# Kernel optimization log

Hardware: AMD Instinct MI355X
Metric: run time of the kernel (lower is better)

Reference implementation:

```python
import math
import jax, jax.numpy as jnp
import numpy as np

GROUPS = 8

def setup_inputs() -> dict:
    key = jax.random.key(0)
    ks = jax.random.split(key, 6)
    N, H, W, C = 8, 128, 128, 512
    s = 1.0 / math.sqrt(C)
    return {
        "x": jax.random.normal(ks[0], (N, H, W, C), dtype=jnp.float32),
        "Wq": jax.random.normal(ks[1], (C, C), dtype=jnp.float32) * s,
        "Wk": jax.random.normal(ks[2], (C, C), dtype=jnp.float32) * s,
        "Wv": jax.random.normal(ks[3], (C, C), dtype=jnp.float32) * s,
        "Wo": jax.random.normal(ks[4], (C, C), dtype=jnp.float32) * s,
        "bo": jnp.zeros((C,), dtype=jnp.float32),
    }

def reference(x, Wq, Wk, Wv, Wo, bo):
    # width=False: attend along H axis -> permute to [N, W, H, C]
    x = jnp.transpose(x, (0, 2, 1, 3))
    N, W, H, C = x.shape
    g = GROUPS
    gp = C // g  # group_planes (head dim)
    xr = x.reshape(N * W, H, C)
    # torch nn.Linear: y = x @ W^T
    q = (xr @ Wq.T).reshape(N * W, H, g, gp)
    k = (xr @ Wk.T).reshape(N * W, H, g, gp)
    v = (xr @ Wv.T).reshape(N * W, H, g, gp)
    attn = jnp.einsum('nigc,njgc->nijg', q, k / math.sqrt(gp))
    attn = jax.nn.softmax(attn, axis=2)
    out = jnp.einsum('nijg,njgc->nigc', attn, v)
    out = out.reshape(N * W, H, C)
    out = out @ Wo.T + bo
    out = out.reshape(N, W, H, C)
    return jnp.transpose(out, (0, 2, 1, 3))
```

## Files before the change

### kernel.cpp

```cpp
#include <hip/hip_runtime.h>
#include <stdint.h>


typedef __attribute__((ext_vector_type(4))) float f32x4;
typedef __attribute__((ext_vector_type(8))) short bf16x8;
typedef unsigned short u16;
typedef unsigned int u32;

#define CBAR() asm volatile("" ::: "memory")
#define SBAR() do { CBAR(); __builtin_amdgcn_s_barrier(); CBAR(); } while(0)
#define LGKM0() do { asm volatile("s_waitcnt lgkmcnt(0)" ::: "memory"); __builtin_amdgcn_sched_barrier(0); } while(0)
#define VMC(n) asm volatile("s_waitcnt vmcnt(" #n ")" ::: "memory")

static __device__ __forceinline__ u16 f2bf(float f){
    union { float f; u32 u; } v; v.f = f;
    u32 r = v.u + 0x7fffu + ((v.u >> 16) & 1u);
    return (u16)(r >> 16);
}

static __device__ __forceinline__ void gload16(const void* g, void* l){
    __builtin_amdgcn_global_load_lds((const __attribute__((address_space(1))) void*)g,
                                     (__attribute__((address_space(3))) void*)l, 16, 0, 0);
}

__global__ void k_wconv(const float* __restrict__ Wq, const float* __restrict__ Wk,
                        const float* __restrict__ Wv, const float* __restrict__ Wo,
                        u16* __restrict__ Wcat, u16* __restrict__ Wob){
    int e = (blockIdx.x * 256 + threadIdx.x) * 4;
    if (e < 1536*512) {
        int row = e >> 9, col = e & 511;
        const float* s = (row < 512) ? (Wq + row*512)
                        : (row < 1024 ? Wk + (row-512)*512 : Wv + (row-1024)*512);
        float4 v = *(const float4*)(s + col);
        ushort4 o = { f2bf(v.x), f2bf(v.y), f2bf(v.z), f2bf(v.w) };
        *(ushort4*)(Wcat + e) = o;
    } else {
        int e2 = e - 1536*512;
        float4 v = *(const float4*)(Wo + e2);
        ushort4 o = { f2bf(v.x), f2bf(v.y), f2bf(v.z), f2bf(v.w) };
        *(ushort4*)(Wob + e2) = o;
    }
}

__global__ void k_xconv(const float* __restrict__ x, u16* __restrict__ xb, int n0){
    int t = blockIdx.x * 256 + threadIdx.x;
    int ml = t >> 6;
    int c0 = (t & 63) << 3;
    int nl = ml >> 7, h = ml & 127;
    int n = n0 + nl, nb = n >> 7, w = n & 127;
    const float* src = x + (size_t)((nb*128 + h)*128 + w) * 512 + c0;
    float4 a = *(const float4*)(src);
    float4 b = *(const float4*)(src + 4);
    uint4 o;
    o.x = (u32)f2bf(a.x) | ((u32)f2bf(a.y) << 16);
    o.y = (u32)f2bf(a.z) | ((u32)f2bf(a.w) << 16);
    o.z = (u32)f2bf(b.x) | ((u32)f2bf(b.y) << 16);
    o.w = (u32)f2bf(b.z) | ((u32)f2bf(b.w) << 16);
    *(uint4*)(xb + (size_t)ml*512 + c0) = o;
}

template<int NCOL, bool OUTPROJ>
__global__ __launch_bounds__(512, 2) void k_gemm4(const u16* __restrict__ A, const u16* __restrict__ B,
                                                  void* __restrict__ Cout, const float* __restrict__ bias,
                                                  int n0, int nrow, int planesz){
    extern __shared__ char smc[];
    const int tid = threadIdx.x;
    const int wid = tid >> 6, lane = tid & 63, lg = lane >> 4, li = lane & 15;
    const int wm = wid >> 2, wn = wid & 3;
    const int bid = blockIdx.x;
    const int xcd = bid & 7, l = bid >> 3;
    const int row_tile = xcd * (nrow >> 3) + l / NCOL;
    const int col_tile = l % NCOL;
    const int m0 = row_tile * 256, nn0 = col_tile * 256;
    const int nbL = row_tile >> 6, h0 = (row_tile & 63) * 2;

    const char* baseA[2]; const char* baseB[2]; int dstR[2];
    #pragma unroll
    for (int i = 0; i < 2; ++i) {
        int R = wid*32 + i*16;
        int r = R + (lane >> 2);
        int cq = (lane & 3) ^ ((r >> 1) & 3);
        long arow;
        if (OUTPROJ) arow = ((long)nbL*128 + (r & 127))*128 + h0 + (r >> 7);
        else         arow = m0 + r;
        baseA[i] = (const char*)(A + (size_t)arow*512) + cq*16;
        baseB[i] = (const char*)(B + (size_t)(nn0 + r)*512) + cq*16;
        dstR[i] = R;
    }
    auto stageA = [&](int st){
        char* sl = smc + (st & 3)*32768;
        #pragma unroll
        for (int i = 0; i < 2; ++i)
            gload16(baseA[i] + st*64, sl + dstR[i]*64);
    };
    auto stageB = [&](int st){
        char* sl = smc + (st & 3)*32768 + 16384;
        #pragma unroll
        for (int i = 0; i < 2; ++i)
            gload16(baseB[i] + st*64, sl + dstR[i]*64);
    };

    f32x4 acc[8][4];
    #pragma unroll
    for (int i = 0; i < 8; ++i)
        #pragma unroll
        for (int j = 0; j < 4; ++j)
            acc[i][j] = f32x4{0.f, 0.f, 0.f, 0.f};

    stageA(0); stageB(0);
    stageA(1); stageB(1);
    stageA(2); stageB(2);
    VMC(8);
    SBAR();

    bf16x8 af[4], bfr[4];
    for (int t = 0; t < 16; ++t) {
        char* sl = smc + (t & 3)*32768;

        #pragma unroll
        for (int f = 0; f < 4; ++f) {
            int ra = wm*128 + f*16 + li;
            af[f] = *(const bf16x8*)(sl + ra*64 + (((lg ^ (ra >> 1)) & 3) << 4));
        }
        #pragma unroll
        for (int f = 0; f < 4; ++f) {
            int rb = wn*64 + f*16 + li;
            bfr[f] = *(const bf16x8*)(sl + 16384 + rb*64 + (((lg ^ (rb >> 1)) & 3) << 4));
        }
        if (t < 13) stageA(t + 3);
        SBAR(); LGKM0();
        __builtin_amdgcn_s_setprio(1);
        #pragma unroll
        for (int fi = 0; fi < 4; ++fi)
            #pragma unroll
            for (int fj = 0; fj < 4; ++fj)
                acc[fi][fj] = __builtin_amdgcn_mfma_f32_16x16x32_bf16(af[fi], bfr[fj], acc[fi][fj], 0, 0, 0);
        __builtin_amdgcn_s_setprio(0);
        SBAR();

        #pragma unroll
        for (int f = 0; f < 4; ++f) {
            int ra = wm*128 + (4 + f)*16 + li;
            af[f] = *(const bf16x8*)(sl + ra*64 + (((lg ^ (ra >> 1)) & 3) << 4));
        }
        if (t < 13) stageB(t + 3);
        SBAR(); LGKM0();
        __builtin_amdgcn_s_setprio(1);
        #pragma unroll
        for (int fi = 0; fi < 4; ++fi)
            #pragma unroll
            for (int fj = 0; fj < 4; ++fj)
                acc[4 + fi][fj] = __builtin_amdgcn_mfma_f32_16x16x32_bf16(af[fi], bfr[fj], acc[4 + fi][fj], 0, 0, 0);
        __builtin_amdgcn_s_setprio(0);
        if (t < 13)      { VMC(8); }
        else if (t == 13){ VMC(4); }
        else if (t == 14){ VMC(0); }
        SBAR();
    }

    if (!OUTPROJ) {
        u16* Cp = (u16*)Cout + (size_t)(nn0 >> 9) * planesz;
        const int cb = (nn0 & 511) + wn*64;
        #pragma unroll
        for (int mf = 0; mf < 8; ++mf)
            #pragma unroll
            for (int nf = 0; nf < 4; ++nf)
                #pragma unroll
                for (int r = 0; r < 4; ++r) {
                    int row = m0 + wm*128 + mf*16 + lg*4 + r;
                    int col = cb + nf*16 + li;
                    Cp[(size_t)row*512 + col] = f2bf(acc[mf][nf][r]);
                }
    } else {
        float* C = (float*)Cout;
        const int nbG = (n0 >> 7) + nbL;
        #pragma unroll
        for (int mf = 0; mf < 8; ++mf)
            #pragma unroll
            for (int nf = 0; nf < 4; ++nf)
                #pragma unroll
                for (int r = 0; r < 4; ++r) {
                    int rho = wm*128 + mf*16 + lg*4 + r;
                    int w = rho & 127, hh = rho >> 7;
                    int col = nn0 + wn*64 + nf*16 + li;
                    size_t orow = (size_t)(nbG*128 + h0 + hh)*128 + w;
                    C[orow*512 + col] = acc[mf][nf][r] + bias[col];
                }
    }
}

__global__ __launch_bounds__(256, 2) void k_attn(const u16* __restrict__ Qpl, const u16* __restrict__ Kpl,
                                                 const u16* __restrict__ Vpl, u16* __restrict__ Ob){
    __shared__ char sm[52224];
    const int g = blockIdx.x;
    const int nl = blockIdx.y;
    const int tid = threadIdx.x;
    const int wid = tid >> 6, lane = tid & 63, lg = lane >> 4, li = lane & 15;

    const u16* Qg = Qpl + (size_t)nl*128*512 + g*64;
    const u16* Kg = Kpl + (size_t)nl*128*512 + g*64;
    const u16* Vg = Vpl + (size_t)nl*128*512 + g*64;
    u16*       Og = Ob  + (size_t)nl*128*512 + g*64;

    #pragma unroll
    for (int it = 0; it < 4; ++it) {
        int gi = it*256 + tid;
        int row = gi >> 3, gs = gi & 7;
        int sw = (gs ^ (row & 7)) << 4;
        gload16((const char*)(Qg + (size_t)row*512) + sw, sm + it*4096 + wid*1024);
        gload16((const char*)(Kg + (size_t)row*512) + sw, sm + 16384 + it*4096 + wid*1024);
    }
    {
        int j = tid & 127, ch = tid >> 7;
        const u16* src = Vg + (size_t)j*512 + ch*32;
        uint4 a0 = *(const uint4*)(src);
        uint4 a1 = *(const uint4*)(src + 8);
        uint4 a2 = *(const uint4*)(src + 16);
        uint4 a3 = *(const uint4*)(src + 24);
        u32 w[16] = {a0.x,a0.y,a0.z,a0.w, a1.x,a1.y,a1.z,a1.w,
                     a2.x,a2.y,a2.z,a2.w, a3.x,a3.y,a3.z,a3.w};
        char* dst = sm + 34816 + ch*32*272 + j*2;
        #pragma unroll
        for (int cc = 0; cc < 32; ++cc) {
            u32 word = w[cc >> 1];
            u16 val = (cc & 1) ? (u16)(word >> 16) : (u16)(word & 0xffffu);
            *(u16*)(dst + cc*272) = val;
        }
    }
    __syncthreads();

    const int i0w = wid*32;
    f32x4 s[2][8];
    #pragma unroll
    for (int t = 0; t < 2; ++t)
        #pragma unroll
        for (int tj = 0; tj < 8; ++tj)
            s[t][tj] = f32x4{0.f,0.f,0.f,0.f};

    #pragma unroll
    for (int ks = 0; ks < 2; ++ks) {
        bf16x8 qf[2];
        #pragma unroll
        for (int t = 0; t < 2; ++t) {
            int ra = i0w + t*16 + li;
            qf[t] = *(const bf16x8*)(sm + ra*128 + ((ks*64 + lg*16) ^ ((ra & 7) << 4)));
        }
        #pragma unroll
        for (int tj = 0; tj < 8; ++tj) {
            int rb = tj*16 + li;
            bf16x8 kf = *(const bf16x8*)(sm + 16384 + rb*128 + ((ks*64 + lg*16) ^ ((rb & 7) << 4)));
            #pragma unroll
            for (int t = 0; t < 2; ++t)
                s[t][tj] = __builtin_amdgcn_mfma_f32_16x16x32_bf16(qf[t], kf, s[t][tj], 0, 0, 0);
        }
    }
    __syncthreads();

    char* pb = sm + wid*8704;
    #pragma unroll
    for (int t = 0; t < 2; ++t) {
        #pragma unroll
        for (int r = 0; r < 4; ++r) {
            float mx = -1e30f;
            #pragma unroll
            for (int tj = 0; tj < 8; ++tj) mx = fmaxf(mx, s[t][tj][r]);
            #pragma unroll
            for (int off = 1; off < 16; off <<= 1) mx = fmaxf(mx, __shfl_xor(mx, off, 64));
            float p[8]; float sum = 0.f;
            #pragma unroll
            for (int tj = 0; tj < 8; ++tj) { p[tj] = __expf((s[t][tj][r] - mx)*0.125f); sum += p[tj]; }
            #pragma unroll
            for (int off = 1; off < 16; off <<= 1) sum += __shfl_xor(sum, off, 64);
            float inv = 1.0f / sum;
            int prow = t*16 + lg*4 + r;
            #pragma unroll
            for (int tj = 0; tj < 8; ++tj)
                *(u16*)(pb + prow*272 + (tj*16 + li)*2) = f2bf(p[tj]*inv);
        }
    }

    f32x4 o[2][4];
    #pragma unroll
    for (int t = 0; t < 2; ++t)
        #pragma unroll
        for (int tc = 0; tc < 4; ++tc)
            o[t][tc] = f32x4{0.f,0.f,0.f,0.f};

    #pragma unroll
    for (int ks = 0; ks < 4; ++ks) {
        bf16x8 pf[2];
        #pragma unroll
        for (int t = 0; t < 2; ++t)
            pf[t] = *(const bf16x8*)(pb + (t*16 + li)*272 + (ks*64 + lg*16));
        #pragma unroll
        for (int tc = 0; tc < 4; ++tc) {
            bf16x8 vf = *(const bf16x8*)(sm + 34816 + (tc*16 + li)*272 + (ks*64 + lg*16));
            #pragma unroll
            for (int t = 0; t < 2; ++t)
                o[t][tc] = __builtin_amdgcn_mfma_f32_16x16x32_bf16(pf[t], vf, o[t][tc], 0, 0, 0);
        }
    }

    #pragma unroll
    for (int t = 0; t < 2; ++t)
        #pragma unroll
        for (int tc = 0; tc < 4; ++tc)
            #pragma unroll
            for (int r = 0; r < 4; ++r) {
                int irow = i0w + t*16 + lg*4 + r;
                int col = tc*16 + li;
                Og[(size_t)irow*512 + col] = f2bf(o[t][tc][r]);
            }
}

extern "C" void kernel_launch(void* const* d_in, const int* in_sizes, int n_in,
                              void* d_out, int out_size, void* d_ws, size_t ws_size,
                              hipStream_t stream){
    const float* x  = (const float*)d_in[0];
    const float* Wq = (const float*)d_in[1];
    const float* Wk = (const float*)d_in[2];
    const float* Wv = (const float*)d_in[3];
    const float* Wo = (const float*)d_in[4];
    const float* bo = (const float*)d_in[5];

    char* ws = (char*)d_ws;
    u16* Wcat = (u16*)ws;
    u16* Wob  = Wcat + 1536*512;

    int CN = 1024;
    while (CN > 128 && (size_t)2097152 + (size_t)CN*524288 > ws_size) CN >>= 1;
    u16* xb   = (u16*)(ws + 2097152);
    u16* QKV2 = xb + (size_t)CN*128*512;
    int planesz = CN*128*512;

    hipFuncSetAttribute((const void*)&k_gemm4<6, false>,
                        hipFuncAttributeMaxDynamicSharedMemorySize, 131072);
    hipFuncSetAttribute((const void*)&k_gemm4<2, true>,
                        hipFuncAttributeMaxDynamicSharedMemorySize, 131072);

    k_wconv<<<1024, 256, 0, stream>>>(Wq, Wk, Wv, Wo, Wcat, Wob);
    int nch = 1024 / CN;
    for (int ch = 0; ch < nch; ++ch) {
        int n0 = ch * CN;
        int nrow = (CN * 128) / 256;
        k_xconv<<<CN*32, 256, 0, stream>>>(x, xb, n0);
        k_gemm4<6, false><<<nrow*6, 512, 131072, stream>>>(xb, Wcat, QKV2, nullptr, 0, nrow, planesz);
        k_attn<<<dim3(8, CN), 256, 0, stream>>>(QKV2, QKV2 + planesz, QKV2 + 2*(size_t)planesz, xb);
        k_gemm4<2, true ><<<nrow*2, 512, 131072, stream>>>(xb, Wob, d_out, bo, n0, nrow, 0);
    }
}
```

Baseline: 615.4 us.

## Fuse attention with output projection into one kernel per sequence

Replaces the separate attention kernel and out-projection GEMM with a single kernel. Each 512-thread block handles one (n,w) sequence, loops over all 8 heads, and keeps the attention output in LDS (128 KB). It then multiplies that output by Wo, streaming Wo tiles through LDS, and writes the fp32 result with bias. This removes the bf16 round trip of the attention output through global memory and one launch. In exchange it uses 160 KB of LDS per block, which limits occupancy to one block per CU, and it re-reads Wo from L2 for every sequence. The Wo loop is serialized with a full wait on every k-chunk.

Result: slower. 653.3 us (+6.2%).

```diff
diff --git a/kernel.cpp b/kernel.cpp
--- a/kernel.cpp
+++ b/kernel.cpp
@@ -10,6 +10,7 @@
 #define CBAR() asm volatile("" ::: "memory")
 #define SBAR() do { CBAR(); __builtin_amdgcn_s_barrier(); CBAR(); } while(0)
 #define LGKM0() do { asm volatile("s_waitcnt lgkmcnt(0)" ::: "memory"); __builtin_amdgcn_sched_barrier(0); } while(0)
+#define LGKMW() asm volatile("s_waitcnt lgkmcnt(0)" ::: "memory")
 #define VMC(n) asm volatile("s_waitcnt vmcnt(" #n ")" ::: "memory")
 
 static __device__ __forceinline__ u16 f2bf(float f){
@@ -59,10 +60,9 @@
     *(uint4*)(xb + (size_t)ml*512 + c0) = o;
 }
 
-template<int NCOL, bool OUTPROJ>
+template<int NCOL>
 __global__ __launch_bounds__(512, 2) void k_gemm4(const u16* __restrict__ A, const u16* __restrict__ B,
-                                                  void* __restrict__ Cout, const float* __restrict__ bias,
-                                                  int n0, int nrow, int planesz){
+                                                  u16* __restrict__ Cout, int nrow, int planesz){
     extern __shared__ char smc[];
     const int tid = threadIdx.x;
     const int wid = tid >> 6, lane = tid & 63, lg = lane >> 4, li = lane & 15;
@@ -72,7 +72,6 @@
     const int row_tile = xcd * (nrow >> 3) + l / NCOL;
     const int col_tile = l % NCOL;
     const int m0 = row_tile * 256, nn0 = col_tile * 256;
-    const int nbL = row_tile >> 6, h0 = (row_tile & 63) * 2;
 
     const char* baseA[2]; const char* baseB[2]; int dstR[2];
     #pragma unroll
@@ -80,24 +79,19 @@
         int R = wid*32 + i*16;
         int r = R + (lane >> 2);
         int cq = (lane & 3) ^ ((r >> 1) & 3);
-        long arow;
-        if (OUTPROJ) arow = ((long)nbL*128 + (r & 127))*128 + h0 + (r >> 7);
-        else         arow = m0 + r;
-        baseA[i] = (const char*)(A + (size_t)arow*512) + cq*16;
+        baseA[i] = (const char*)(A + (size_t)(m0 + r)*512) + cq*16;
         baseB[i] = (const char*)(B + (size_t)(nn0 + r)*512) + cq*16;
         dstR[i] = R;
     }
     auto stageA = [&](int st){
         char* sl = smc + (st & 3)*32768;
         #pragma unroll
-        for (int i = 0; i < 2; ++i)
-            gload16(baseA[i] + st*64, sl + dstR[i]*64);
+        for (int i = 0; i < 2; ++i) gload16(baseA[i] + st*64, sl + dstR[i]*64);
     };
     auto stageB = [&](int st){
         char* sl = smc + (st & 3)*32768 + 16384;
         #pragma unroll
-        for (int i = 0; i < 2; ++i)
-            gload16(baseB[i] + st*64, sl + dstR[i]*64);
+        for (int i = 0; i < 2; ++i) gload16(baseB[i] + st*64, sl + dstR[i]*64);
     };
 
     f32x4 acc[8][4];
@@ -116,7 +110,6 @@
     bf16x8 af[4], bfr[4];
     for (int t = 0; t < 16; ++t) {
         char* sl = smc + (t & 3)*32768;
-
         #pragma unroll
         for (int f = 0; f < 4; ++f) {
             int ra = wm*128 + f*16 + li;
@@ -137,7 +130,6 @@
                 acc[fi][fj] = __builtin_amdgcn_mfma_f32_16x16x32_bf16(af[fi], bfr[fj], acc[fi][fj], 0, 0, 0);
         __builtin_amdgcn_s_setprio(0);
         SBAR();
-
         #pragma unroll
         for (int f = 0; f < 4; ++f) {
             int ra = wm*128 + (4 + f)*16 + li;
@@ -158,159 +150,191 @@
         SBAR();
     }
 
-    if (!OUTPROJ) {
-        u16* Cp = (u16*)Cout + (size_t)(nn0 >> 9) * planesz;
-        const int cb = (nn0 & 511) + wn*64;
-        #pragma unroll
-        for (int mf = 0; mf < 8; ++mf)
-            #pragma unroll
-            for (int nf = 0; nf < 4; ++nf)
-                #pragma unroll
-                for (int r = 0; r < 4; ++r) {
-                    int row = m0 + wm*128 + mf*16 + lg*4 + r;
-                    int col = cb + nf*16 + li;
-                    Cp[(size_t)row*512 + col] = f2bf(acc[mf][nf][r]);
-                }
-    } else {
-        float* C = (float*)Cout;
-        const int nbG = (n0 >> 7) + nbL;
-        #pragma unroll
-        for (int mf = 0; mf < 8; ++mf)
-            #pragma unroll
-            for (int nf = 0; nf < 4; ++nf)
-                #pragma unroll
-                for (int r = 0; r < 4; ++r) {
-                    int rho = wm*128 + mf*16 + lg*4 + r;
-                    int w = rho & 127, hh = rho >> 7;
-                    int col = nn0 + wn*64 + nf*16 + li;
-                    size_t orow = (size_t)(nbG*128 + h0 + hh)*128 + w;
-                    C[orow*512 + col] = acc[mf][nf][r] + bias[col];
-                }
-    }
-}
-
-__global__ __launch_bounds__(256, 2) void k_attn(const u16* __restrict__ Qpl, const u16* __restrict__ Kpl,
-                                                 const u16* __restrict__ Vpl, u16* __restrict__ Ob){
-    __shared__ char sm[52224];
-    const int g = blockIdx.x;
-    const int nl = blockIdx.y;
+    u16* Cp = Cout + (size_t)(nn0 >> 9) * planesz;
+    const int cb = (nn0 & 511) + wn*64;
+    #pragma unroll
+    for (int mf = 0; mf < 8; ++mf)
+        #pragma unroll
+        for (int nf = 0; nf < 4; ++nf)
+            #pragma unroll
+            for (int r = 0; r < 4; ++r) {
+                int row = m0 + wm*128 + mf*16 + lg*4 + r;
+                int col = cb + nf*16 + li;
+                Cp[(size_t)row*512 + col] = f2bf(acc[mf][nf][r]);
+            }
+}
+
+__global__ __launch_bounds__(512, 2) void k_fused(const u16* __restrict__ Qpl, const u16* __restrict__ Kpl,
+                                                  const u16* __restrict__ Vpl, const u16* __restrict__ Wob,
+                                                  const float* __restrict__ bias, float* __restrict__ out,
+                                                  int n0, int cnd8){
+    extern __shared__ char sm[];
     const int tid = threadIdx.x;
-    const int wid = tid >> 6, lane = tid & 63, lg = lane >> 4, li = lane & 15;
-
-    const u16* Qg = Qpl + (size_t)nl*128*512 + g*64;
-    const u16* Kg = Kpl + (size_t)nl*128*512 + g*64;
-    const u16* Vg = Vpl + (size_t)nl*128*512 + g*64;
-    u16*       Og = Ob  + (size_t)nl*128*512 + g*64;
-
-    #pragma unroll
-    for (int it = 0; it < 4; ++it) {
-        int gi = it*256 + tid;
-        int row = gi >> 3, gs = gi & 7;
-        int sw = (gs ^ (row & 7)) << 4;
-        gload16((const char*)(Qg + (size_t)row*512) + sw, sm + it*4096 + wid*1024);
-        gload16((const char*)(Kg + (size_t)row*512) + sw, sm + 16384 + it*4096 + wid*1024);
-    }
-    {
-        int j = tid & 127, ch = tid >> 7;
-        const u16* src = Vg + (size_t)j*512 + ch*32;
-        uint4 a0 = *(const uint4*)(src);
-        uint4 a1 = *(const uint4*)(src + 8);
-        uint4 a2 = *(const uint4*)(src + 16);
-        uint4 a3 = *(const uint4*)(src + 24);
-        u32 w[16] = {a0.x,a0.y,a0.z,a0.w, a1.x,a1.y,a1.z,a1.w,
-                     a2.x,a2.y,a2.z,a2.w, a3.x,a3.y,a3.z,a3.w};
-        char* dst = sm + 34816 + ch*32*272 + j*2;
-        #pragma unroll
-        for (int cc = 0; cc < 32; ++cc) {
-            u32 word = w[cc >> 1];
-            u16 val = (cc & 1) ? (u16)(word >> 16) : (u16)(word & 0xffffu);
-            *(u16*)(dst + cc*272) = val;
-        }
-    }
-    __syncthreads();
-
-    const int i0w = wid*32;
-    f32x4 s[2][8];
-    #pragma unroll
-    for (int t = 0; t < 2; ++t)
-        #pragma unroll
-        for (int tj = 0; tj < 8; ++tj)
-            s[t][tj] = f32x4{0.f,0.f,0.f,0.f};
-
-    #pragma unroll
-    for (int ks = 0; ks < 2; ++ks) {
-        bf16x8 qf[2];
+    const int wv = tid >> 6, lane = tid & 63, lg = lane >> 4, li = lane & 15;
+    const int bid = blockIdx.x;
+    const int nlL = (bid & 7)*cnd8 + (bid >> 3);
+    const int n = n0 + nlL, nb = n >> 7, w = n & 127;
+
+    char* const QB = sm + 131072;
+    char* const KB = sm + 131072 + 16384;
+    char* const PB = sm + 131072 + wv*4096;
+    char* const SB = sm + 131072;
+
+    const int vj = tid & 127, vch = tid >> 7;
+    const size_t rowbase = (size_t)nlL * 128;
+
+    auto issueQK = [&](int g){
         #pragma unroll
         for (int t = 0; t < 2; ++t) {
-            int ra = i0w + t*16 + li;
-            qf[t] = *(const bf16x8*)(sm + ra*128 + ((ks*64 + lg*16) ^ ((ra & 7) << 4)));
-        }
-        #pragma unroll
-        for (int tj = 0; tj < 8; ++tj) {
-            int rb = tj*16 + li;
-            bf16x8 kf = *(const bf16x8*)(sm + 16384 + rb*128 + ((ks*64 + lg*16) ^ ((rb & 7) << 4)));
-            #pragma unroll
-            for (int t = 0; t < 2; ++t)
-                s[t][tj] = __builtin_amdgcn_mfma_f32_16x16x32_bf16(qf[t], kf, s[t][tj], 0, 0, 0);
-        }
-    }
-    __syncthreads();
-
-    char* pb = sm + wid*8704;
-    #pragma unroll
-    for (int t = 0; t < 2; ++t) {
+            int i = t*64 + (tid >> 3);
+            int cq = (tid & 7) ^ (i & 7);
+            gload16(Qpl + (rowbase + i)*512 + g*64 + cq*8, QB + t*8192 + tid*16);
+            gload16(Kpl + (rowbase + i)*512 + g*64 + cq*8, KB + t*8192 + tid*16);
+        }
+    };
+
+    uint4 va, vb;
+    auto issueV = [&](int g){
+        const u16* src = Vpl + (rowbase + vj)*512 + g*64 + vch*16;
+        va = *(const uint4*)(src);
+        vb = *(const uint4*)(src + 8);
+    };
+
+    issueQK(0);
+    issueV(0);
+    __builtin_amdgcn_sched_barrier(0);
+
+    for (int g = 0; g < 8; ++g) {
+        char* OG = sm + g*16384;
+
+        VMC(0);
+        SBAR();
+
+        f32x4 s8[8];
+        #pragma unroll
+        for (int tj = 0; tj < 8; ++tj) s8[tj] = f32x4{0.f,0.f,0.f,0.f};
+        #pragma unroll
+        for (int ks = 0; ks < 2; ++ks) {
+            int i = wv*16 + li;
+            bf16x8 qf = *(const bf16x8*)(QB + i*128 + ((ks*64 + lg*16) ^ ((li & 7) << 4)));
+            #pragma unroll
+            for (int tj = 0; tj < 8; ++tj) {
+                int j = tj*16 + li;
+                bf16x8 kf = *(const bf16x8*)(KB + j*128 + ((ks*64 + lg*16) ^ ((li & 7) << 4)));
+                s8[tj] = __builtin_amdgcn_mfma_f32_16x16x32_bf16(qf, kf, s8[tj], 0, 0, 0);
+            }
+        }
+
+        {
+            u32 wd[8] = {va.x, va.y, va.z, va.w, vb.x, vb.y, vb.z, vb.w};
+            #pragma unroll
+            for (int cc = 0; cc < 16; ++cc) {
+                int c = vch*16 + cc;
+                u16 val = (cc & 1) ? (u16)(wd[cc >> 1] >> 16) : (u16)(wd[cc >> 1] & 0xffffu);
+                *(u16*)(OG + c*256 + ((vj*2) ^ ((c & 7) << 4))) = val;
+            }
+        }
+
+        SBAR();
+
         #pragma unroll
         for (int r = 0; r < 4; ++r) {
+            int ir = lg*4 + r;
             float mx = -1e30f;
             #pragma unroll
-            for (int tj = 0; tj < 8; ++tj) mx = fmaxf(mx, s[t][tj][r]);
+            for (int tj = 0; tj < 8; ++tj) mx = fmaxf(mx, s8[tj][r]);
             #pragma unroll
             for (int off = 1; off < 16; off <<= 1) mx = fmaxf(mx, __shfl_xor(mx, off, 64));
             float p[8]; float sum = 0.f;
             #pragma unroll
-            for (int tj = 0; tj < 8; ++tj) { p[tj] = __expf((s[t][tj][r] - mx)*0.125f); sum += p[tj]; }
+            for (int tj = 0; tj < 8; ++tj) { p[tj] = __expf((s8[tj][r] - mx)*0.125f); sum += p[tj]; }
             #pragma unroll
             for (int off = 1; off < 16; off <<= 1) sum += __shfl_xor(sum, off, 64);
             float inv = 1.0f / sum;
-            int prow = t*16 + lg*4 + r;
-            #pragma unroll
-            for (int tj = 0; tj < 8; ++tj)
-                *(u16*)(pb + prow*272 + (tj*16 + li)*2) = f2bf(p[tj]*inv);
-        }
-    }
-
-    f32x4 o[2][4];
-    #pragma unroll
-    for (int t = 0; t < 2; ++t)
+            #pragma unroll
+            for (int tj = 0; tj < 8; ++tj) {
+                int j = tj*16 + li;
+                *(u16*)(PB + ir*256 + ((j*2) ^ ((ir & 7) << 4))) = f2bf(p[tj]*inv);
+            }
+        }
+
+        LGKMW();
+        SBAR();
+
+        f32x4 o4[4];
+        #pragma unroll
+        for (int tc = 0; tc < 4; ++tc) o4[tc] = f32x4{0.f,0.f,0.f,0.f};
+        #pragma unroll
+        for (int ks = 0; ks < 4; ++ks) {
+            bf16x8 pf = *(const bf16x8*)(PB + li*256 + ((ks*64 + lg*16) ^ ((li & 7) << 4)));
+            #pragma unroll
+            for (int tc = 0; tc < 4; ++tc) {
+                int c = tc*16 + li;
+                bf16x8 vf = *(const bf16x8*)(OG + c*256 + ((ks*64 + lg*16) ^ ((c & 7) << 4)));
+                o4[tc] = __builtin_amdgcn_mfma_f32_16x16x32_bf16(pf, vf, o4[tc], 0, 0, 0);
+            }
+        }
+
+        SBAR();
+
+        if (g < 7) {
+            issueQK(g + 1);
+            issueV(g + 1);
+            __builtin_amdgcn_sched_barrier(0);
+        }
+
         #pragma unroll
         for (int tc = 0; tc < 4; ++tc)
-            o[t][tc] = f32x4{0.f,0.f,0.f,0.f};
-
-    #pragma unroll
-    for (int ks = 0; ks < 4; ++ks) {
-        bf16x8 pf[2];
-        #pragma unroll
-        for (int t = 0; t < 2; ++t)
-            pf[t] = *(const bf16x8*)(pb + (t*16 + li)*272 + (ks*64 + lg*16));
-        #pragma unroll
-        for (int tc = 0; tc < 4; ++tc) {
-            bf16x8 vf = *(const bf16x8*)(sm + 34816 + (tc*16 + li)*272 + (ks*64 + lg*16));
-            #pragma unroll
-            for (int t = 0; t < 2; ++t)
-                o[t][tc] = __builtin_amdgcn_mfma_f32_16x16x32_bf16(pf[t], vf, o[t][tc], 0, 0, 0);
-        }
-    }
-
-    #pragma unroll
-    for (int t = 0; t < 2; ++t)
-        #pragma unroll
-        for (int tc = 0; tc < 4; ++tc)
             #pragma unroll
             for (int r = 0; r < 4; ++r) {
-                int irow = i0w + t*16 + lg*4 + r;
-                int col = tc*16 + li;
-                Og[(size_t)irow*512 + col] = f2bf(o[t][tc][r]);
-            }
+                int i = wv*16 + lg*4 + r;
+                int c = tc*16 + li;
+                *(u16*)(OG + i*128 + ((c*2) ^ ((i & 7) << 4))) = f2bf(o4[tc][r]);
+            }
+    }
+
+    LGKMW();
+
+    float br[32];
+    #pragma unroll
+    for (int cf = 0; cf < 32; ++cf) br[cf] = bias[cf*16 + li];
+
+    f32x4 y[32];
+    #pragma unroll
+    for (int cf = 0; cf < 32; ++cf) y[cf] = f32x4{0.f,0.f,0.f,0.f};
+
+    for (int kc = 0; kc < 16; ++kc) {
+        #pragma unroll
+        for (int p = 0; p < 4; ++p) {
+            int co = p*128 + (tid >> 2);
+            int cq = (tid & 3) ^ ((co >> 1) & 3);
+            gload16(Wob + (size_t)co*512 + kc*32 + cq*8, SB + p*8192 + tid*16);
+        }
+        VMC(0); LGKMW();
+        SBAR();
+
+        int i = wv*16 + li;
+        bf16x8 af = *(const bf16x8*)(sm + (kc >> 1)*16384 + i*128 +
+                                     (((kc & 1)*64 + lg*16) ^ ((li & 7) << 4)));
+        __builtin_amdgcn_s_setprio(1);
+        #pragma unroll
+        for (int cf = 0; cf < 32; ++cf) {
+            int co = cf*16 + li;
+            bf16x8 bf = *(const bf16x8*)(SB + co*64 + ((lg << 4) ^ (((co >> 1) & 3) << 4)));
+            y[cf] = __builtin_amdgcn_mfma_f32_16x16x32_bf16(af, bf, y[cf], 0, 0, 0);
+        }
+        __builtin_amdgcn_s_setprio(0);
+        SBAR();
+    }
+
+    #pragma unroll
+    for (int cf = 0; cf < 32; ++cf)
+        #pragma unroll
+        for (int r = 0; r < 4; ++r) {
+            int i = wv*16 + lg*4 + r;
+            int co = cf*16 + li;
+            out[((size_t)(nb*128 + i)*128 + w)*512 + co] = y[cf][r] + br[cf];
+        }
 }
 
 extern "C" void kernel_launch(void* const* d_in, const int* in_sizes, int n_in,
@@ -333,10 +357,10 @@
     u16* QKV2 = xb + (size_t)CN*128*512;
     int planesz = CN*128*512;
 
-    hipFuncSetAttribute((const void*)&k_gemm4<6, false>,
+    hipFuncSetAttribute((const void*)&k_gemm4<6>,
                         hipFuncAttributeMaxDynamicSharedMemorySize, 131072);
-    hipFuncSetAttribute((const void*)&k_gemm4<2, true>,
-                        hipFuncAttributeMaxDynamicSharedMemorySize, 131072);
+    hipFuncSetAttribute((const void*)&k_fused,
+                        hipFuncAttributeMaxDynamicSharedMemorySize, 163840);
 
     k_wconv<<<1024, 256, 0, stream>>>(Wq, Wk, Wv, Wo, Wcat, Wob);
     int nch = 1024 / CN;
@@ -344,8 +368,8 @@
         int n0 = ch * CN;
         int nrow = (CN * 128) / 256;
         k_xconv<<<CN*32, 256, 0, stream>>>(x, xb, n0);
-        k_gemm4<6, false><<<nrow*6, 512, 131072, stream>>>(xb, Wcat, QKV2, nullptr, 0, nrow, planesz);
-        k_attn<<<dim3(8, CN), 256, 0, stream>>>(QKV2, QKV2 + planesz, QKV2 + 2*(size_t)planesz, xb);
-        k_gemm4<2, true ><<<nrow*2, 512, 131072, stream>>>(xb, Wob, d_out, bo, n0, nrow, 0);
-    }
-}
+        k_gemm4<6><<<nrow*6, 512, 131072, stream>>>(xb, Wcat, QKV2, nrow, planesz);
+        k_fused<<<CN, 512, 163840, stream>>>(QKV2, QKV2 + planesz, QKV2 + 2*(size_t)planesz,
+                                             Wob, bo, (float*)d_out, n0, CN/8);
+    }
+}
```
